# Kernel tuning notes

Hardware: AMD Instinct MI355X
Metric: run time of the kernel (lower is better)

Reference implementation:

```python
import jax, jax.numpy as jnp
import numpy as np

N = 50000      # nodes per graph
E = 800000     # edges per graph
IN_DIM = 64
HIDDEN = 128
OUT_DIM = 2
P = 100000     # candidate residue pairs


def setup_inputs() -> dict:
    key = jax.random.key(0)
    ks = jax.random.split(key, 12)
    x1 = jax.random.normal(ks[0], (N, IN_DIM), dtype=jnp.float32)
    x2 = jax.random.normal(ks[1], (N, IN_DIM), dtype=jnp.float32)
    edge_index1 = jax.random.randint(ks[2], (2, E), 0, N, dtype=jnp.int64)
    edge_index2 = jax.random.randint(ks[3], (2, E), 0, N, dtype=jnp.int64)
    label = jax.random.randint(ks[4], (P, 2), 0, N, dtype=jnp.int64)
    s = 0.05
    W0 = jax.random.normal(ks[5], (IN_DIM, HIDDEN), dtype=jnp.float32) * s
    W1 = jax.random.normal(ks[6], (HIDDEN, HIDDEN), dtype=jnp.float32) * s
    W2 = jax.random.normal(ks[7], (HIDDEN, HIDDEN), dtype=jnp.float32) * s
    b0 = jnp.zeros((HIDDEN,), dtype=jnp.float32)
    b1 = jnp.zeros((HIDDEN,), dtype=jnp.float32)
    b2 = jnp.zeros((HIDDEN,), dtype=jnp.float32)
    fcW = jax.random.normal(ks[8], (2 * HIDDEN, OUT_DIM), dtype=jnp.float32) * s
    fcb = jnp.zeros((OUT_DIM,), dtype=jnp.float32)
    return {"x1": x1, "edge_index1": edge_index1, "x2": x2,
            "edge_index2": edge_index2, "label": label,
            "W0": W0, "b0": b0, "W1": W1, "b1": b1, "W2": W2, "b2": b2,
            "fcW": fcW, "fcb": fcb}


def gcn_conv(x, src, dst, W, b):
    """PyG GCNConv: linear, add self-loops, symmetric D^-1/2 (A+I) D^-1/2 aggregation."""
    n = x.shape[0]
    h = x @ W                                   # [n, out]
    loops = jnp.arange(n, dtype=src.dtype)
    src_sl = jnp.concatenate([src, loops])      # [E+n]
    dst_sl = jnp.concatenate([dst, loops])
    deg = jax.ops.segment_sum(jnp.ones_like(src_sl, dtype=h.dtype), dst_sl,
                              num_segments=n)
    dinv = jax.lax.rsqrt(jnp.maximum(deg, 1.0e-12))
    norm = dinv[src_sl] * dinv[dst_sl]          # [E+n]
    msgs = h[src_sl] * norm[:, None]            # gather + scale
    out = jax.ops.segment_sum(msgs, dst_sl, num_segments=n)  # scatter-add
    return out + b


def gcn_tower(x, edge_index, params):
    src, dst = edge_index[0], edge_index[1]
    for (W, b) in params:
        x = jax.nn.relu(gcn_conv(x, src, dst, W, b))
    return x


def reference(x1, edge_index1, x2, edge_index2, label,
              W0, b0, W1, b1, W2, b2, fcW, fcb):
    params = [(W0, b0), (W1, b1), (W2, b2)]
    x_ligand = gcn_tower(x1, edge_index1, params)    # shared GCN weights
    x_receptor = gcn_tower(x2, edge_index2, params)
    x = jnp.concatenate([x_ligand[label[:, 0]], x_receptor[label[:, 1]]], axis=1)
    return jax.nn.relu(x @ fcW + fcb)
```

## Files before the change

kernel.cpp:

```cpp
#include <hip/hip_runtime.h>
#include <math.h>

typedef __attribute__((ext_vector_type(8))) short bf16x8;
typedef __attribute__((ext_vector_type(4))) float f32x4;

__device__ inline unsigned short f2bf(float f) {
    unsigned int u = __float_as_uint(f);
    unsigned int r = u + 0x7fffu + ((u >> 16) & 1u);
    return (unsigned short)(r >> 16);
}
__device__ inline float bf2f(unsigned short b) {
    return __uint_as_float(((unsigned int)b) << 16);
}


__global__ void histU_kernel(const int* __restrict__ d1, const int* __restrict__ d2,
                             int* __restrict__ cnt, int E, int N) {
    int i = blockIdx.x * blockDim.x + threadIdx.x;
    if (i < E) atomicAdd(&cnt[d1[i]], 1);
    else if (i < 2 * E) atomicAdd(&cnt[N + d2[i - E]], 1);
}

__global__ __launch_bounds__(256) void block_reduce_kernel(const int* __restrict__ cnt,
                                                           float* __restrict__ dinv,
                                                           int* __restrict__ blockSums, int NN) {
    int i = blockIdx.x * 256 + threadIdx.x;
    int v = 0;
    if (i < NN) {
        v = cnt[i];
        dinv[i] = 1.0f / sqrtf((float)(v + 1));
    }
    int s = v;
#pragma unroll
    for (int o = 32; o; o >>= 1) s += __shfl_down(s, o);
    __shared__ int ws[4];
    if ((threadIdx.x & 63) == 0) ws[threadIdx.x >> 6] = s;
    __syncthreads();
    if (threadIdx.x == 0) blockSums[blockIdx.x] = ws[0] + ws[1] + ws[2] + ws[3];
}

__global__ __launch_bounds__(1024) void scan_sums_kernel(const int* __restrict__ blockSums,
                                                         int* __restrict__ blockOff, int nb,
                                                         int* __restrict__ rowptr, int NN) {
    __shared__ int sh[1024];
    int t = threadIdx.x;
    int v = (t < nb) ? blockSums[t] : 0;
    sh[t] = v;
    __syncthreads();
    for (int o = 1; o < 1024; o <<= 1) {
        int u = (t >= o) ? sh[t - o] : 0;
        __syncthreads();
        sh[t] += u;
        __syncthreads();
    }
    if (t < nb) blockOff[t] = sh[t] - v;
    if (t == 1023) rowptr[NN] = sh[1023];
}

__global__ __launch_bounds__(256) void scan_write_kernel(const int* __restrict__ cnt,
                                                         const int* __restrict__ blockOff,
                                                         int* __restrict__ rowptr, int NN) {
    __shared__ int sh[256];
    int i = blockIdx.x * 256 + threadIdx.x;
    int t = threadIdx.x;
    int v = (i < NN) ? cnt[i] : 0;
    sh[t] = v;
    __syncthreads();
    for (int o = 1; o < 256; o <<= 1) {
        int u = (t >= o) ? sh[t - o] : 0;
        __syncthreads();
        sh[t] += u;
        __syncthreads();
    }
    if (i < NN) rowptr[i] = blockOff[blockIdx.x] + sh[t] - v;
}

__global__ void placeU_kernel(const int* __restrict__ s1, const int* __restrict__ d1,
                              const int* __restrict__ s2, const int* __restrict__ d2,
                              const int* __restrict__ rowptr, int* __restrict__ cnt,
                              int* __restrict__ csr, int E, int N) {
    int i = blockIdx.x * blockDim.x + threadIdx.x;
    int s, d;
    if (i < E)          { s = s1[i];         d = d1[i]; }
    else if (i < 2 * E) { s = s2[i - E] + N; d = d2[i - E] + N; }
    else return;
    int p = atomicSub(&cnt[d], 1);
    csr[rowptr[d] + p - 1] = s;
}


__global__ void prep_weights(const float* __restrict__ W0, const float* __restrict__ W1,
                             const float* __restrict__ W2,
                             unsigned short* __restrict__ W0h, unsigned short* __restrict__ W0l,
                             unsigned short* __restrict__ W1h, unsigned short* __restrict__ W1l,
                             unsigned short* __restrict__ W2h, unsigned short* __restrict__ W2l) {
    const float* W; unsigned short *Wh, *Wl; int K;
    if (blockIdx.x == 0)      { W = W0; Wh = W0h; Wl = W0l; K = 64; }
    else if (blockIdx.x == 1) { W = W1; Wh = W1h; Wl = W1l; K = 128; }
    else                      { W = W2; Wh = W2h; Wl = W2l; K = 128; }
    for (int i = threadIdx.x; i < K * 128; i += 256) {
        int k = i >> 7, c = i & 127;
        float v = W[i];
        unsigned short h = f2bf(v);
        unsigned short l = f2bf(v - bf2f(h));
        Wh[c * K + k] = h;
        Wl[c * K + k] = l;
    }
}


__global__ void agg64U_kernel(const float* __restrict__ x1, const float* __restrict__ x2,
                              const int* __restrict__ rowptr, const int* __restrict__ csr,
                              const float* __restrict__ dinv,
                              unsigned short* __restrict__ Shi, unsigned short* __restrict__ Slo,
                              int NN, int N) {
    int w = blockIdx.x * (blockDim.x >> 6) + (threadIdx.x >> 6);
    int lane = threadIdx.x & 63;
    if (w >= NN) return;
    int beg = rowptr[w], end = rowptr[w + 1];
    const float* selfrow = (w < N) ? (x1 + (size_t)w * 64) : (x2 + (size_t)(w - N) * 64);
    float acc = dinv[w] * selfrow[lane];
    int e = beg;
    int full_end = beg + ((end - beg) & ~7);
    for (; e < full_end; e += 8) {
        int s0 = csr[e], s1 = csr[e + 1], s2 = csr[e + 2], s3 = csr[e + 3];
        int s4 = csr[e + 4], s5 = csr[e + 5], s6 = csr[e + 6], s7 = csr[e + 7];
        const float* r0 = (s0 < N) ? (x1 + (size_t)s0 * 64) : (x2 + (size_t)(s0 - N) * 64);
        const float* r1 = (s1 < N) ? (x1 + (size_t)s1 * 64) : (x2 + (size_t)(s1 - N) * 64);
        const float* r2 = (s2 < N) ? (x1 + (size_t)s2 * 64) : (x2 + (size_t)(s2 - N) * 64);
        const float* r3 = (s3 < N) ? (x1 + (size_t)s3 * 64) : (x2 + (size_t)(s3 - N) * 64);
        const float* r4 = (s4 < N) ? (x1 + (size_t)s4 * 64) : (x2 + (size_t)(s4 - N) * 64);
        const float* r5 = (s5 < N) ? (x1 + (size_t)s5 * 64) : (x2 + (size_t)(s5 - N) * 64);
        const float* r6 = (s6 < N) ? (x1 + (size_t)s6 * 64) : (x2 + (size_t)(s6 - N) * 64);
        const float* r7 = (s7 < N) ? (x1 + (size_t)s7 * 64) : (x2 + (size_t)(s7 - N) * 64);
        float v0 = dinv[s0] * r0[lane];
        float v1 = dinv[s1] * r1[lane];
        float v2 = dinv[s2] * r2[lane];
        float v3 = dinv[s3] * r3[lane];
        float v4 = dinv[s4] * r4[lane];
        float v5 = dinv[s5] * r5[lane];
        float v6 = dinv[s6] * r6[lane];
        float v7 = dinv[s7] * r7[lane];
        acc += ((v0 + v1) + (v2 + v3)) + ((v4 + v5) + (v6 + v7));
    }
    if (e < end) {
#pragma unroll
        for (int j = 0; j < 7; ++j) {
            int a = e + j;
            bool vld = a < end;
            int s = csr[vld ? a : beg];
            float wt = vld ? dinv[s] : 0.f;
            const float* r = (s < N) ? (x1 + (size_t)s * 64) : (x2 + (size_t)(s - N) * 64);
            acc += wt * r[lane];
        }
    }
    unsigned short h = f2bf(acc);
    Shi[(size_t)w * 64 + lane] = h;
    Slo[(size_t)w * 64 + lane] = f2bf(acc - bf2f(h));
}


__global__ void agg128_kernel(const float* __restrict__ Xf, const int* __restrict__ rowptr,
                              const int* __restrict__ csr,
                              unsigned short* __restrict__ Shi, unsigned short* __restrict__ Slo,
                              int NN) {
    int w = blockIdx.x * (blockDim.x >> 6) + (threadIdx.x >> 6);
    int lane = threadIdx.x & 63;
    if (w >= NN) return;
    const float2* X = (const float2*)Xf;
    int beg = rowptr[w], end = rowptr[w + 1];
    float2 self = X[(size_t)w * 64 + lane];
    float ax = self.x, ay = self.y;
    int e = beg;
    int full_end = beg + ((end - beg) & ~7);
    for (; e < full_end; e += 8) {
        int s0 = csr[e], s1 = csr[e + 1], s2 = csr[e + 2], s3 = csr[e + 3];
        int s4 = csr[e + 4], s5 = csr[e + 5], s6 = csr[e + 6], s7 = csr[e + 7];
        float2 v0 = X[(size_t)s0 * 64 + lane];
        float2 v1 = X[(size_t)s1 * 64 + lane];
        float2 v2 = X[(size_t)s2 * 64 + lane];
        float2 v3 = X[(size_t)s3 * 64 + lane];
        float2 v4 = X[(size_t)s4 * 64 + lane];
        float2 v5 = X[(size_t)s5 * 64 + lane];
        float2 v6 = X[(size_t)s6 * 64 + lane];
        float2 v7 = X[(size_t)s7 * 64 + lane];
        ax += ((v0.x + v1.x) + (v2.x + v3.x)) + ((v4.x + v5.x) + (v6.x + v7.x));
        ay += ((v0.y + v1.y) + (v2.y + v3.y)) + ((v4.y + v5.y) + (v6.y + v7.y));
    }
    if (e < end) {
#pragma unroll
        for (int j = 0; j < 7; ++j) {
            int a = e + j;
            bool vld = a < end;
            int s = csr[vld ? a : beg];
            float m = vld ? 1.f : 0.f;
            float2 v = X[(size_t)s * 64 + lane];
            ax += m * v.x; ay += m * v.y;
        }
    }
    unsigned short hx = f2bf(ax), hy = f2bf(ay);
    ushort2 H; H.x = hx; H.y = hy;
    ushort2 L; L.x = f2bf(ax - bf2f(hx)); L.y = f2bf(ay - bf2f(hy));
    *reinterpret_cast<ushort2*>(Shi + (size_t)w * 128 + 2 * lane) = H;
    *reinterpret_cast<ushort2*>(Slo + (size_t)w * 128 + 2 * lane) = L;
}


template <int K>
__global__ __launch_bounds__(512) void gemm_mfma(const unsigned short* __restrict__ Ah,
                                                 const unsigned short* __restrict__ Al,
                                                 const unsigned short* __restrict__ WhT,
                                                 const unsigned short* __restrict__ WlT,
                                                 const float* __restrict__ bias,
                                                 const float* __restrict__ dinv, int post,
                                                 float* __restrict__ C, int M) {
    const int LDA = K + 8;
    __shared__ unsigned short lds[2 * 128 * LDA];
    unsigned short* ldsH = lds;
    unsigned short* ldsL = lds + 128 * LDA;

    int t = threadIdx.x;
    int lane = t & 63, wid = t >> 6;
    int c16 = lane & 15, kq = (lane >> 4) * 8;
    int row0 = blockIdx.x * 128;

    bf16x8 wh[K / 32], wl[K / 32];
    {
        int col = wid * 16 + c16;
#pragma unroll
        for (int ks = 0; ks < K / 32; ++ks) {
            wh[ks] = *reinterpret_cast<const bf16x8*>(WhT + (size_t)col * K + ks * 32 + kq);
            wl[ks] = *reinterpret_cast<const bf16x8*>(WlT + (size_t)col * K + ks * 32 + kq);
        }
    }

    const int CH = 128 * K / 8;
    for (int c = t; c < CH; c += 512) {
        int row = c / (K / 8), kb = c % (K / 8);
        int gr = row0 + row; if (gr >= M) gr = M - 1;
        *reinterpret_cast<bf16x8*>(ldsH + row * LDA + kb * 8) =
            *reinterpret_cast<const bf16x8*>(Ah + (size_t)gr * K + kb * 8);
        *reinterpret_cast<bf16x8*>(ldsL + row * LDA + kb * 8) =
            *reinterpret_cast<const bf16x8*>(Al + (size_t)gr * K + kb * 8);
    }
    __syncthreads();

    float bb = bias[wid * 16 + c16];
#pragma unroll
    for (int rt = 0; rt < 8; ++rt) {
        f32x4 acc = {0.f, 0.f, 0.f, 0.f};
        int abase = (rt * 16 + c16) * LDA + kq;
#pragma unroll
        for (int ks = 0; ks < K / 32; ++ks) {
            bf16x8 ah = *reinterpret_cast<const bf16x8*>(ldsH + abase + ks * 32);
            bf16x8 al = *reinterpret_cast<const bf16x8*>(ldsL + abase + ks * 32);
            acc = __builtin_amdgcn_mfma_f32_16x16x32_bf16(ah, wh[ks], acc, 0, 0, 0);
            acc = __builtin_amdgcn_mfma_f32_16x16x32_bf16(ah, wl[ks], acc, 0, 0, 0);
            acc = __builtin_amdgcn_mfma_f32_16x16x32_bf16(al, wh[ks], acc, 0, 0, 0);
        }
#pragma unroll
        for (int r = 0; r < 4; ++r) {
            int gr = row0 + rt * 16 + (lane >> 4) * 4 + r;
            if (gr < M) {
                float d = dinv[gr];
                float po = post ? d : 1.0f;
                float v = fmaxf(acc[r] * d + bb, 0.f) * po;
                C[(size_t)gr * 128 + wid * 16 + c16] = v;
            }
        }
    }
}


__global__ void fc_kernel(const float* __restrict__ H3, const int* __restrict__ label,
                          const float* __restrict__ fcW, const float* __restrict__ fcb,
                          float* __restrict__ out, int P, int N) {
    int w = blockIdx.x * (blockDim.x >> 6) + (threadIdx.x >> 6);
    int lane = threadIdx.x & 63;
    if (w >= P) return;
    int l0 = label[2 * w], l1 = label[2 * w + 1] + N;
    float xl0 = H3[(size_t)l0 * 128 + lane];
    float xl1 = H3[(size_t)l0 * 128 + 64 + lane];
    float xr0 = H3[(size_t)l1 * 128 + lane];
    float xr1 = H3[(size_t)l1 * 128 + 64 + lane];
    float a0 = xl0 * fcW[lane * 2]             + xl1 * fcW[(64 + lane) * 2]
             + xr0 * fcW[(128 + lane) * 2]     + xr1 * fcW[(192 + lane) * 2];
    float a1 = xl0 * fcW[lane * 2 + 1]         + xl1 * fcW[(64 + lane) * 2 + 1]
             + xr0 * fcW[(128 + lane) * 2 + 1] + xr1 * fcW[(192 + lane) * 2 + 1];
#pragma unroll
    for (int o = 32; o; o >>= 1) {
        a0 += __shfl_xor(a0, o);
        a1 += __shfl_xor(a1, o);
    }
    if (lane == 0) {
        out[2 * w]     = fmaxf(a0 + fcb[0], 0.f);
        out[2 * w + 1] = fmaxf(a1 + fcb[1], 0.f);
    }
}


extern "C" void kernel_launch(void* const* d_in, const int* in_sizes, int n_in,
                              void* d_out, int out_size, void* d_ws, size_t ws_size,
                              hipStream_t stream) {
    const float* x1   = (const float*)d_in[0];
    const int*   e1   = (const int*)d_in[1];
    const float* x2   = (const float*)d_in[2];
    const int*   e2   = (const int*)d_in[3];
    const int*   label= (const int*)d_in[4];
    const float* W0   = (const float*)d_in[5];
    const float* b0   = (const float*)d_in[6];
    const float* W1   = (const float*)d_in[7];
    const float* b1   = (const float*)d_in[8];
    const float* W2   = (const float*)d_in[9];
    const float* b2   = (const float*)d_in[10];
    const float* fcW  = (const float*)d_in[11];
    const float* fcb  = (const float*)d_in[12];
    float* out = (float*)d_out;

    const int N = in_sizes[0] / 64;
    const int E = in_sizes[1] / 2;
    const int P = in_sizes[4] / 2;
    const int NN = 2 * N;
    const int NB = (NN + 255) / 256;

    char* ws = (char*)d_ws;
    size_t off = 0;
    auto alloc = [&](size_t bytes) -> void* {
        void* p = ws + off;
        off += (bytes + 255) & ~(size_t)255;
        return p;
    };
    int*   cnt      = (int*)alloc((size_t)NN * 4);
    int*   rowptr   = (int*)alloc((size_t)(NN + 1) * 4);
    float* dinv     = (float*)alloc((size_t)NN * 4);
    int*   csr      = (int*)alloc((size_t)2 * E * 4);
    int*   blockSums= (int*)alloc((size_t)NB * 4);
    int*   blockOff = (int*)alloc((size_t)NB * 4);
    unsigned short* Shi = (unsigned short*)alloc((size_t)NN * 128 * 2);
    unsigned short* Slo = (unsigned short*)alloc((size_t)NN * 128 * 2);
    float* Xs       = (float*)alloc((size_t)NN * 128 * 4);
    unsigned short* W0h = (unsigned short*)alloc(64 * 128 * 2);
    unsigned short* W0l = (unsigned short*)alloc(64 * 128 * 2);
    unsigned short* W1h = (unsigned short*)alloc(128 * 128 * 2);
    unsigned short* W1l = (unsigned short*)alloc(128 * 128 * 2);
    unsigned short* W2h = (unsigned short*)alloc(128 * 128 * 2);
    unsigned short* W2l = (unsigned short*)alloc(128 * 128 * 2);

    const int GB = (NN + 127) / 128;

    prep_weights<<<3, 256, 0, stream>>>(W0, W1, W2, W0h, W0l, W1h, W1l, W2h, W2l);

    hipMemsetAsync(cnt, 0, (size_t)NN * 4, stream);
    histU_kernel<<<(2 * E + 255) / 256, 256, 0, stream>>>(e1 + E, e2 + E, cnt, E, N);
    block_reduce_kernel<<<NB, 256, 0, stream>>>(cnt, dinv, blockSums, NN);
    scan_sums_kernel<<<1, 1024, 0, stream>>>(blockSums, blockOff, NB, rowptr, NN);
    scan_write_kernel<<<NB, 256, 0, stream>>>(cnt, blockOff, rowptr, NN);
    placeU_kernel<<<(2 * E + 255) / 256, 256, 0, stream>>>(e1, e1 + E, e2, e2 + E,
                                                           rowptr, cnt, csr, E, N);
    agg64U_kernel<<<(NN + 3) / 4, 256, 0, stream>>>(x1, x2, rowptr, csr, dinv, Shi, Slo, NN, N);
    gemm_mfma<64><<<GB, 512, 0, stream>>>(Shi, Slo, W0h, W0l, b0, dinv, 1, Xs, NN);
    agg128_kernel<<<(NN + 3) / 4, 256, 0, stream>>>(Xs, rowptr, csr, Shi, Slo, NN);
    gemm_mfma<128><<<GB, 512, 0, stream>>>(Shi, Slo, W1h, W1l, b1, dinv, 1, Xs, NN);
    agg128_kernel<<<(NN + 3) / 4, 256, 0, stream>>>(Xs, rowptr, csr, Shi, Slo, NN);
    gemm_mfma<128><<<GB, 512, 0, stream>>>(Shi, Slo, W2h, W2l, b2, dinv, 0, Xs, NN);

    fc_kernel<<<(P + 3) / 4, 256, 0, stream>>>(Xs, label, fcW, fcb, out, P, N);
}
```

Baseline: 584.6 us.

## Store features in 8-wide column slices and aggregate per slice

After: 1.960 ms. 3.35x slower.

```diff
diff --git a/kernel.cpp b/kernel.cpp
--- a/kernel.cpp
+++ b/kernel.cpp
@@ -109,100 +109,71 @@
 }
 
 
-__global__ void agg64U_kernel(const float* __restrict__ x1, const float* __restrict__ x2,
-                              const int* __restrict__ rowptr, const int* __restrict__ csr,
-                              const float* __restrict__ dinv,
-                              unsigned short* __restrict__ Shi, unsigned short* __restrict__ Slo,
-                              int NN, int N) {
-    int w = blockIdx.x * (blockDim.x >> 6) + (threadIdx.x >> 6);
-    int lane = threadIdx.x & 63;
-    if (w >= NN) return;
-    int beg = rowptr[w], end = rowptr[w + 1];
-    const float* selfrow = (w < N) ? (x1 + (size_t)w * 64) : (x2 + (size_t)(w - N) * 64);
-    float acc = dinv[w] * selfrow[lane];
-    int e = beg;
-    int full_end = beg + ((end - beg) & ~7);
-    for (; e < full_end; e += 8) {
-        int s0 = csr[e], s1 = csr[e + 1], s2 = csr[e + 2], s3 = csr[e + 3];
-        int s4 = csr[e + 4], s5 = csr[e + 5], s6 = csr[e + 6], s7 = csr[e + 7];
-        const float* r0 = (s0 < N) ? (x1 + (size_t)s0 * 64) : (x2 + (size_t)(s0 - N) * 64);
-        const float* r1 = (s1 < N) ? (x1 + (size_t)s1 * 64) : (x2 + (size_t)(s1 - N) * 64);
-        const float* r2 = (s2 < N) ? (x1 + (size_t)s2 * 64) : (x2 + (size_t)(s2 - N) * 64);
-        const float* r3 = (s3 < N) ? (x1 + (size_t)s3 * 64) : (x2 + (size_t)(s3 - N) * 64);
-        const float* r4 = (s4 < N) ? (x1 + (size_t)s4 * 64) : (x2 + (size_t)(s4 - N) * 64);
-        const float* r5 = (s5 < N) ? (x1 + (size_t)s5 * 64) : (x2 + (size_t)(s5 - N) * 64);
-        const float* r6 = (s6 < N) ? (x1 + (size_t)s6 * 64) : (x2 + (size_t)(s6 - N) * 64);
-        const float* r7 = (s7 < N) ? (x1 + (size_t)s7 * 64) : (x2 + (size_t)(s7 - N) * 64);
-        float v0 = dinv[s0] * r0[lane];
-        float v1 = dinv[s1] * r1[lane];
-        float v2 = dinv[s2] * r2[lane];
-        float v3 = dinv[s3] * r3[lane];
-        float v4 = dinv[s4] * r4[lane];
-        float v5 = dinv[s5] * r5[lane];
-        float v6 = dinv[s6] * r6[lane];
-        float v7 = dinv[s7] * r7[lane];
-        acc += ((v0 + v1) + (v2 + v3)) + ((v4 + v5) + (v6 + v7));
-    }
-    if (e < end) {
-#pragma unroll
-        for (int j = 0; j < 7; ++j) {
-            int a = e + j;
-            bool vld = a < end;
-            int s = csr[vld ? a : beg];
-            float wt = vld ? dinv[s] : 0.f;
-            const float* r = (s < N) ? (x1 + (size_t)s * 64) : (x2 + (size_t)(s - N) * 64);
-            acc += wt * r[lane];
-        }
-    }
-    unsigned short h = f2bf(acc);
-    Shi[(size_t)w * 64 + lane] = h;
-    Slo[(size_t)w * 64 + lane] = f2bf(acc - bf2f(h));
-}
-
-
-__global__ void agg128_kernel(const float* __restrict__ Xf, const int* __restrict__ rowptr,
-                              const int* __restrict__ csr,
-                              unsigned short* __restrict__ Shi, unsigned short* __restrict__ Slo,
-                              int NN) {
-    int w = blockIdx.x * (blockDim.x >> 6) + (threadIdx.x >> 6);
-    int lane = threadIdx.x & 63;
-    if (w >= NN) return;
-    const float2* X = (const float2*)Xf;
-    int beg = rowptr[w], end = rowptr[w + 1];
-    float2 self = X[(size_t)w * 64 + lane];
-    float ax = self.x, ay = self.y;
-    int e = beg;
-    int full_end = beg + ((end - beg) & ~7);
-    for (; e < full_end; e += 8) {
-        int s0 = csr[e], s1 = csr[e + 1], s2 = csr[e + 2], s3 = csr[e + 3];
-        int s4 = csr[e + 4], s5 = csr[e + 5], s6 = csr[e + 6], s7 = csr[e + 7];
-        float2 v0 = X[(size_t)s0 * 64 + lane];
-        float2 v1 = X[(size_t)s1 * 64 + lane];
-        float2 v2 = X[(size_t)s2 * 64 + lane];
-        float2 v3 = X[(size_t)s3 * 64 + lane];
-        float2 v4 = X[(size_t)s4 * 64 + lane];
-        float2 v5 = X[(size_t)s5 * 64 + lane];
-        float2 v6 = X[(size_t)s6 * 64 + lane];
-        float2 v7 = X[(size_t)s7 * 64 + lane];
-        ax += ((v0.x + v1.x) + (v2.x + v3.x)) + ((v4.x + v5.x) + (v6.x + v7.x));
-        ay += ((v0.y + v1.y) + (v2.y + v3.y)) + ((v4.y + v5.y) + (v6.y + v7.y));
-    }
-    if (e < end) {
-#pragma unroll
-        for (int j = 0; j < 7; ++j) {
-            int a = e + j;
-            bool vld = a < end;
-            int s = csr[vld ? a : beg];
-            float m = vld ? 1.f : 0.f;
-            float2 v = X[(size_t)s * 64 + lane];
-            ax += m * v.x; ay += m * v.y;
-        }
-    }
-    unsigned short hx = f2bf(ax), hy = f2bf(ay);
-    ushort2 H; H.x = hx; H.y = hy;
-    ushort2 L; L.x = f2bf(ax - bf2f(hx)); L.y = f2bf(ay - bf2f(hy));
-    *reinterpret_cast<ushort2*>(Shi + (size_t)w * 128 + 2 * lane) = H;
-    *reinterpret_cast<ushort2*>(Slo + (size_t)w * 128 + 2 * lane) = L;
+__global__ __launch_bounds__(256) void xpose_kernel(const float* __restrict__ x1,
+                                                    const float* __restrict__ x2,
+                                                    const float* __restrict__ dinv,
+                                                    float* __restrict__ X0sl, int NN, int N) {
+    int t = threadIdx.x;
+    int node = blockIdx.x * 32 + (t >> 3);
+    int sf = t & 7;
+    if (node >= NN) return;
+    const float* xr = (node < N) ? (x1 + (size_t)node * 64) : (x2 + (size_t)(node - N) * 64);
+    float d = dinv[node];
+    float4 a = *reinterpret_cast<const float4*>(xr + sf * 8);
+    float4 b = *reinterpret_cast<const float4*>(xr + sf * 8 + 4);
+    a.x *= d; a.y *= d; a.z *= d; a.w *= d;
+    b.x *= d; b.y *= d; b.z *= d; b.w *= d;
+    float* o = X0sl + ((size_t)sf * NN + node) * 8;
+    *reinterpret_cast<float4*>(o) = a;
+    *reinterpret_cast<float4*>(o + 4) = b;
+}
+
+
+__global__ __launch_bounds__(256) void agg_slice_kernel(
+    const float* __restrict__ Xsl, const int* __restrict__ rowptr,
+    const int* __restrict__ csr,
+    unsigned short* __restrict__ Shi, unsigned short* __restrict__ Slo,
+    int NN, int nchunks) {
+    int b = blockIdx.x;
+    int sgroup = b / (8 * nchunks);
+    int rem = b - sgroup * 8 * nchunks;
+    int slice = (rem & 7) + 8 * sgroup;
+    int chunk = rem >> 3;
+    int t = threadIdx.x;
+    int feat = t & 7;
+    int g = t >> 3;
+
+    const float* Xs = Xsl + (size_t)slice * NN * 8;
+    unsigned short* Hh = Shi + (size_t)slice * NN * 8;
+    unsigned short* Hl = Slo + (size_t)slice * NN * 8;
+
+    for (int it = 0; it < 512; it += 32) {
+        int base = chunk * 512 + it;
+        if (base >= NN) break;
+        int node = base + g;
+        bool alive = node < NN;
+        int beg = 0, deg = 0;
+        if (alive) {
+            beg = rowptr[node];
+            deg = rowptr[node + 1] - beg;
+        }
+        float acc = alive ? Xs[(size_t)node * 8 + feat] : 0.f;
+        for (int k = 0; k < deg; k += 8) {
+#pragma unroll
+            for (int j = 0; j < 8; ++j) {
+                int idx = k + j;
+                if (idx < deg) {
+                    int s = __builtin_nontemporal_load(csr + beg + idx);
+                    acc += Xs[(size_t)s * 8 + feat];
+                }
+            }
+        }
+        if (alive) {
+            unsigned short h = f2bf(acc);
+            Hh[(size_t)node * 8 + feat] = h;
+            Hl[(size_t)node * 8 + feat] = f2bf(acc - bf2f(h));
+        }
+    }
 }
 
 
@@ -212,42 +183,40 @@
                                                  const unsigned short* __restrict__ WhT,
                                                  const unsigned short* __restrict__ WlT,
                                                  const float* __restrict__ bias,
-                                                 const float* __restrict__ dinv, int post,
+                                                 const float* __restrict__ dinv, int mode,
                                                  float* __restrict__ C, int M) {
     const int LDA = K + 8;
-    __shared__ unsigned short lds[2 * 128 * LDA];
-    unsigned short* ldsH = lds;
-    unsigned short* ldsL = lds + 128 * LDA;
+    __shared__ unsigned short ldsH[64 * LDA];
+    __shared__ unsigned short ldsL[64 * LDA];
 
     int t = threadIdx.x;
     int lane = t & 63, wid = t >> 6;
     int c16 = lane & 15, kq = (lane >> 4) * 8;
-    int row0 = blockIdx.x * 128;
+    int row0 = blockIdx.x * 64;
+    int col = wid * 16 + c16;
 
     bf16x8 wh[K / 32], wl[K / 32];
-    {
-        int col = wid * 16 + c16;
-#pragma unroll
-        for (int ks = 0; ks < K / 32; ++ks) {
-            wh[ks] = *reinterpret_cast<const bf16x8*>(WhT + (size_t)col * K + ks * 32 + kq);
-            wl[ks] = *reinterpret_cast<const bf16x8*>(WlT + (size_t)col * K + ks * 32 + kq);
-        }
-    }
-
-    const int CH = 128 * K / 8;
+#pragma unroll
+    for (int ks = 0; ks < K / 32; ++ks) {
+        wh[ks] = *reinterpret_cast<const bf16x8*>(WhT + (size_t)col * K + ks * 32 + kq);
+        wl[ks] = *reinterpret_cast<const bf16x8*>(WlT + (size_t)col * K + ks * 32 + kq);
+    }
+
+    const int CH = 64 * (K / 8);
     for (int c = t; c < CH; c += 512) {
-        int row = c / (K / 8), kb = c % (K / 8);
+        int row = c & 63, sf = c >> 6;
         int gr = row0 + row; if (gr >= M) gr = M - 1;
-        *reinterpret_cast<bf16x8*>(ldsH + row * LDA + kb * 8) =
-            *reinterpret_cast<const bf16x8*>(Ah + (size_t)gr * K + kb * 8);
-        *reinterpret_cast<bf16x8*>(ldsL + row * LDA + kb * 8) =
-            *reinterpret_cast<const bf16x8*>(Al + (size_t)gr * K + kb * 8);
+        size_t ga = ((size_t)sf * M + gr) * 8;
+        *reinterpret_cast<bf16x8*>(&ldsH[row * LDA + sf * 8]) =
+            *reinterpret_cast<const bf16x8*>(Ah + ga);
+        *reinterpret_cast<bf16x8*>(&ldsL[row * LDA + sf * 8]) =
+            *reinterpret_cast<const bf16x8*>(Al + ga);
     }
     __syncthreads();
 
-    float bb = bias[wid * 16 + c16];
-#pragma unroll
-    for (int rt = 0; rt < 8; ++rt) {
+    float bb = bias[col];
+#pragma unroll
+    for (int rt = 0; rt < 4; ++rt) {
         f32x4 acc = {0.f, 0.f, 0.f, 0.f};
         int abase = (rt * 16 + c16) * LDA + kq;
 #pragma unroll
@@ -263,9 +232,13 @@
             int gr = row0 + rt * 16 + (lane >> 4) * 4 + r;
             if (gr < M) {
                 float d = dinv[gr];
-                float po = post ? d : 1.0f;
-                float v = fmaxf(acc[r] * d + bb, 0.f) * po;
-                C[(size_t)gr * 128 + wid * 16 + c16] = v;
+                if (mode) {
+                    float v = fmaxf(acc[r] * d + bb, 0.f) * d;
+                    C[((size_t)(col >> 3) * M + gr) * 8 + (col & 7)] = v;
+                } else {
+                    float v = fmaxf(acc[r] * d + bb, 0.f);
+                    C[(size_t)gr * 128 + col] = v;
+                }
             }
         }
     }
@@ -322,6 +295,8 @@
     const int P = in_sizes[4] / 2;
     const int NN = 2 * N;
     const int NB = (NN + 255) / 256;
+    const int NCH = (NN + 511) / 512;
+    const int GB = (NN + 63) / 64;
 
     char* ws = (char*)d_ws;
     size_t off = 0;
@@ -336,17 +311,15 @@
     int*   csr      = (int*)alloc((size_t)2 * E * 4);
     int*   blockSums= (int*)alloc((size_t)NB * 4);
     int*   blockOff = (int*)alloc((size_t)NB * 4);
+    float* regA     = (float*)alloc((size_t)NN * 128 * 4);
     unsigned short* Shi = (unsigned short*)alloc((size_t)NN * 128 * 2);
     unsigned short* Slo = (unsigned short*)alloc((size_t)NN * 128 * 2);
-    float* Xs       = (float*)alloc((size_t)NN * 128 * 4);
     unsigned short* W0h = (unsigned short*)alloc(64 * 128 * 2);
     unsigned short* W0l = (unsigned short*)alloc(64 * 128 * 2);
     unsigned short* W1h = (unsigned short*)alloc(128 * 128 * 2);
     unsigned short* W1l = (unsigned short*)alloc(128 * 128 * 2);
     unsigned short* W2h = (unsigned short*)alloc(128 * 128 * 2);
     unsigned short* W2l = (unsigned short*)alloc(128 * 128 * 2);
-
-    const int GB = (NN + 127) / 128;
 
     prep_weights<<<3, 256, 0, stream>>>(W0, W1, W2, W0h, W0l, W1h, W1l, W2h, W2l);
 
@@ -357,12 +330,13 @@
     scan_write_kernel<<<NB, 256, 0, stream>>>(cnt, blockOff, rowptr, NN);
     placeU_kernel<<<(2 * E + 255) / 256, 256, 0, stream>>>(e1, e1 + E, e2, e2 + E,
                                                            rowptr, cnt, csr, E, N);
-    agg64U_kernel<<<(NN + 3) / 4, 256, 0, stream>>>(x1, x2, rowptr, csr, dinv, Shi, Slo, NN, N);
-    gemm_mfma<64><<<GB, 512, 0, stream>>>(Shi, Slo, W0h, W0l, b0, dinv, 1, Xs, NN);
-    agg128_kernel<<<(NN + 3) / 4, 256, 0, stream>>>(Xs, rowptr, csr, Shi, Slo, NN);
-    gemm_mfma<128><<<GB, 512, 0, stream>>>(Shi, Slo, W1h, W1l, b1, dinv, 1, Xs, NN);
-    agg128_kernel<<<(NN + 3) / 4, 256, 0, stream>>>(Xs, rowptr, csr, Shi, Slo, NN);
-    gemm_mfma<128><<<GB, 512, 0, stream>>>(Shi, Slo, W2h, W2l, b2, dinv, 0, Xs, NN);
-
-    fc_kernel<<<(P + 3) / 4, 256, 0, stream>>>(Xs, label, fcW, fcb, out, P, N);
-}
+    xpose_kernel<<<(NN + 31) / 32, 256, 0, stream>>>(x1, x2, dinv, regA, NN, N);
+    agg_slice_kernel<<<8 * NCH, 256, 0, stream>>>(regA, rowptr, csr, Shi, Slo, NN, NCH);
+    gemm_mfma<64><<<GB, 512, 0, stream>>>(Shi, Slo, W0h, W0l, b0, dinv, 1, regA, NN);
+    agg_slice_kernel<<<16 * NCH, 256, 0, stream>>>(regA, rowptr, csr, Shi, Slo, NN, NCH);
+    gemm_mfma<128><<<GB, 512, 0, stream>>>(Shi, Slo, W1h, W1l, b1, dinv, 1, regA, NN);
+    agg_slice_kernel<<<16 * NCH, 256, 0, stream>>>(regA, rowptr, csr, Shi, Slo, NN, NCH);
+    gemm_mfma<128><<<GB, 512, 0, stream>>>(Shi, Slo, W2h, W2l, b2, dinv, 0, regA, NN);
+
+    fc_kernel<<<(P + 3) / 4, 256, 0, stream>>>(regA, label, fcW, fcb, out, P, N);
+}
```
